# Optimization experiments

Measured on AMD Instinct MI355X. Metric: run time of the kernel, lower is better.

Reference implementation:

```python
import jax, jax.numpy as jnp
import numpy as np
from jax import lax

EPS = 1e-5
K = 16  # MixedOp.self.k


def conv(x, w, stride=1, pad=0, dil=1, groups=1):
    return lax.conv_general_dilated(
        x, w, (stride, stride), [(pad, pad), (pad, pad)],
        rhs_dilation=(dil, dil), feature_group_count=groups,
        dimension_numbers=('NCHW', 'OIHW', 'NCHW'))


def bn(x):
    # BatchNorm2d(affine=False) in training mode: normalize with batch stats
    m = jnp.mean(x, axis=(0, 2, 3), keepdims=True)
    v = jnp.var(x, axis=(0, 2, 3), keepdims=True)
    return (x - m) * lax.rsqrt(v + EPS)


def maxpool3(x):
    return lax.reduce_window(x, -jnp.inf, lax.max, (1, 1, 3, 3), (1, 1, 1, 1),
                             [(0, 0), (0, 0), (1, 1), (1, 1)])


def avgpool3(x):
    # AvgPool2d(3, stride=1, padding=1, count_include_pad=False)
    s = lax.reduce_window(x, 0., lax.add, (1, 1, 3, 3), (1, 1, 1, 1),
                          [(0, 0), (0, 0), (1, 1), (1, 1)])
    c = lax.reduce_window(jnp.ones_like(x), 0., lax.add, (1, 1, 3, 3),
                          (1, 1, 1, 1), [(0, 0), (0, 0), (1, 1), (1, 1)])
    return s / c


def sep_conv(x, dw1, pw1, dw2, pw2):
    C = x.shape[1]
    p = dw1.shape[-1] // 2
    h = jax.nn.relu(x)
    h = conv(h, dw1, pad=p, groups=C)
    h = bn(conv(h, pw1))
    h = jax.nn.relu(h)
    h = conv(h, dw2, pad=p, groups=C)
    return bn(conv(h, pw2))


def dil_conv(x, dw, pw):
    C = x.shape[1]
    p = (dw.shape[-1] // 2) * 2  # dilation=2 padding (3x3->2, 5x5->4)
    h = jax.nn.relu(x)
    h = conv(h, dw, pad=p, dil=2, groups=C)
    return bn(conv(h, pw))


def setup_inputs() -> dict:
    key = jax.random.key(0)
    C, B, H, W = 256, 32, 64, 64
    c_op = C // K  # 16 channels fed to each candidate op
    ks = jax.random.split(key, 17)
    g = lambda k, shp, fan: jax.random.normal(k, shp, jnp.float32) / np.sqrt(fan)
    return {
        'x': jax.random.normal(ks[0], (B, C, H, W), jnp.float32),
        # ChannelAttention se: 1x1 convs, reduction=2
        'ca_w1': g(ks[1], (C // 2, C, 1, 1), C),
        'ca_w2': g(ks[2], (C, C // 2, 1, 1), C // 2),
        # sep_conv_3x3 (two dw+pw stages)
        's3_dw1': g(ks[3], (c_op, 1, 3, 3), 9),
        's3_pw1': g(ks[4], (c_op, c_op, 1, 1), c_op),
        's3_dw2': g(ks[5], (c_op, 1, 3, 3), 9),
        's3_pw2': g(ks[6], (c_op, c_op, 1, 1), c_op),
        # sep_conv_5x5
        's5_dw1': g(ks[7], (c_op, 1, 5, 5), 25),
        's5_pw1': g(ks[8], (c_op, c_op, 1, 1), c_op),
        's5_dw2': g(ks[9], (c_op, 1, 5, 5), 25),
        's5_pw2': g(ks[10], (c_op, c_op, 1, 1), c_op),
        # dil_conv_3x3 / dil_conv_5x5
        'd3_dw': g(ks[11], (c_op, 1, 3, 3), 9),
        'd3_pw': g(ks[12], (c_op, c_op, 1, 1), c_op),
        'd5_dw': g(ks[13], (c_op, 1, 5, 5), 25),
        'd5_pw': g(ks[14], (c_op, c_op, 1, 1), c_op),
        # AttentionModule fc: channel = 8*c_op = 128, ratio = 8
        'at_w1': g(ks[15], (c_op, 8 * c_op), 8 * c_op),  # Linear(128->16)
        'at_w2': g(ks[16], (8 * c_op, c_op), c_op),      # Linear(16->128)
    }


def reference(x, ca_w1, ca_w2, s3_dw1, s3_pw1, s3_dw2, s3_pw2,
              s5_dw1, s5_pw1, s5_dw2, s5_pw2, d3_dw, d3_pw, d5_dw, d5_pw,
              at_w1, at_w2):
    B, C, H, W = x.shape
    c_sel = C // K  # number of selected channels (16)

    # ---- ChannelAttention ----
    mx = jnp.max(x, axis=(2, 3), keepdims=True)   # [B,C,1,1]
    av = jnp.mean(x, axis=(2, 3), keepdims=True)
    se = lambda z: conv(jax.nn.relu(conv(z, ca_w1)), ca_w2)
    num_list = jax.nn.sigmoid(se(mx) + se(av))    # [B,C,1,1]

    aux = x                                       # auxiliary_op = Identity (stride=1)
    xg = x * num_list

    # ---- top-k channel routing ----
    slist = jnp.sum(num_list, axis=0).reshape(C)  # sum over batch
    _, idx = lax.top_k(slist, c_sel)              # sorted, largest first
    xt = xg[:, idx]                               # gather [B,c_sel,H,W]

    # ---- 8 candidate branches (DARTS PRIMITIVES, stride=1) ----
    branches = [
        jnp.zeros_like(xt),                       # none
        bn(maxpool3(xt)),                         # max_pool_3x3 + BN
        bn(avgpool3(xt)),                         # avg_pool_3x3 + BN
        xt,                                       # skip_connect (Identity)
        sep_conv(xt, s3_dw1, s3_pw1, s3_dw2, s3_pw2),
        sep_conv(xt, s5_dw1, s5_pw1, s5_dw2, s5_pw2),
        dil_conv(xt, d3_dw, d3_pw),
        dil_conv(xt, d5_dw, d5_pw),
    ]
    temp = jnp.concatenate(branches, axis=1)      # [B, 8*c_sel, H, W]

    # ---- AttentionModule ----
    y = jnp.mean(temp, axis=(2, 3))               # [B, 8*c_sel]
    y = jax.nn.sigmoid(jax.nn.relu(y @ at_w1.T) @ at_w2.T)
    att = temp * y[:, :, None, None]
    op_attention = jnp.sum(y.reshape(B, 8, c_sel), axis=(0, 2))  # [8]

    # sum the 8 branch chunks
    out = jnp.sum(att.reshape(B, 8, c_sel, H, W), axis=1)

    # scatter back into gated x, then residual add
    xg = xg.at[:, idx].set(out)
    return xg + aux, op_attention
```

## Files before the change

### kernel.cpp

```cpp
#include <hip/hip_runtime.h>
#include <math.h>

static constexpr int B = 32, C = 256, HW = 4096, CS = 16;
static constexpr int BHW = B * HW;
static constexpr size_t IMG = (size_t)B * CS * HW;

static constexpr size_t OFF_S    = 0;
static constexpr size_t OFF_SQ   = 4096;
static constexpr size_t OFF_U    = 8192;
static constexpr size_t OFF_CNT  = 8256;
static constexpr size_t ACC_END  = 8260;
static constexpr size_t OFF_MX   = 8320;
static constexpr size_t OFF_AV   = OFF_MX + 8192;
static constexpr size_t OFF_NUM  = OFF_AV + 8192;
static constexpr size_t OFF_Y    = OFF_NUM + 8192;
static constexpr size_t OFF_ACO  = OFF_Y + 4096;
static constexpr size_t OFF_BIAS = OFF_ACO + 4096;
static constexpr size_t OFF_INT  = OFF_BIAS + 512;
static constexpr size_t OFF_R    = OFF_INT + 384;

__device__ inline float wave_sum(float v) {
  v += __shfl_down(v, 32); v += __shfl_down(v, 16); v += __shfl_down(v, 8);
  v += __shfl_down(v, 4);  v += __shfl_down(v, 2);  v += __shfl_down(v, 1);
  return v;
}
__device__ inline float wave_max(float v) {
  v = fmaxf(v, __shfl_down(v, 32)); v = fmaxf(v, __shfl_down(v, 16));
  v = fmaxf(v, __shfl_down(v, 8));  v = fmaxf(v, __shfl_down(v, 4));
  v = fmaxf(v, __shfl_down(v, 2));  v = fmaxf(v, __shfl_down(v, 1));
  return v;
}

__global__ __launch_bounds__(256) void k_stats(const float4* __restrict__ x,
                                               float* __restrict__ mx, float* __restrict__ av,
                                               float* __restrict__ accbase) {
  int bc = blockIdx.x;
  if (bc == 0) for (int i = threadIdx.x; i < (int)ACC_END; i += 256) accbase[i] = 0.f;
  const float4* p = x + (size_t)bc * 1024;
  float mmax = -INFINITY, msum = 0.f;
  for (int i = threadIdx.x; i < 1024; i += 256) {
    float4 v = p[i];
    mmax = fmaxf(mmax, fmaxf(fmaxf(v.x, v.y), fmaxf(v.z, v.w)));
    msum += v.x + v.y + v.z + v.w;
  }
  __shared__ float rs[4], rm[4];
  float s = wave_sum(msum), m = wave_max(mmax);
  int w = threadIdx.x >> 6;
  if ((threadIdx.x & 63) == 0) { rs[w] = s; rm[w] = m; }
  __syncthreads();
  if (threadIdx.x == 0) {
    mx[bc] = fmaxf(fmaxf(rm[0], rm[1]), fmaxf(rm[2], rm[3]));
    av[bc] = (rs[0] + rs[1] + rs[2] + rs[3]) * (1.f / 4096.f);
  }
}

__global__ __launch_bounds__(256) void k_sesel(const float* __restrict__ mx, const float* __restrict__ av,
                                               const float* __restrict__ w1, const float* __restrict__ w2,
                                               float* __restrict__ num,
                                               int* __restrict__ idx, int* __restrict__ selmap,
                                               unsigned* __restrict__ cnt) {
  __shared__ float zs0[256], zs1[256], h0[128], h1[128];
  __shared__ unsigned lastv;
  int b = blockIdx.x, t = threadIdx.x;
  zs0[t] = mx[b * 256 + t]; zs1[t] = av[b * 256 + t];
  __syncthreads();
  if (t < 128) {
    const float* wr = w1 + (size_t)t * 256;
    float am = 0.f, aa = 0.f;
    for (int i = 0; i < 256; i++) { float w = wr[i]; am = fmaf(w, zs0[i], am); aa = fmaf(w, zs1[i], aa); }
    h0[t] = fmaxf(am, 0.f); h1[t] = fmaxf(aa, 0.f);
  }
  __syncthreads();
  {
    const float* wr = w2 + (size_t)t * 128;
    float sm = 0.f, sa = 0.f;
    for (int j = 0; j < 128; j++) { float w = wr[j]; sm = fmaf(w, h0[j], sm); sa = fmaf(w, h1[j], sa); }
    num[b * 256 + t] = 1.f / (1.f + expf(-(sm + sa)));
  }
  __threadfence();
  if (t == 0) lastv = atomicAdd(cnt, 1u);
  __syncthreads();
  if (lastv == 31u) {
    __threadfence();
    float acc = 0.f;
    for (int bb = 0; bb < B; bb++) acc += num[bb * 256 + t];
    zs0[t] = acc; selmap[t] = -1;
    __syncthreads();
    float v = zs0[t];
    int rank = 0;
    for (int c = 0; c < 256; c++) {
      float o = zs0[c];
      rank += (o > v) || (o == v && c < t);
    }
    if (rank < 16) { idx[rank] = t; selmap[t] = rank; }
  }
}

__global__ __launch_bounds__(256) void k_fuseA(
    const float* __restrict__ x, const float* __restrict__ num, const int* __restrict__ idx,
    const float* __restrict__ d3dw, const float* __restrict__ d5dw,
    const float* __restrict__ s3dw1, const float* __restrict__ s5dw1,
    float* __restrict__ R, float* __restrict__ scr,
    float* __restrict__ S, float* __restrict__ SQ) {
  __shared__ float lt[72 * 72];
  __shared__ float red[20];
  const int t = threadIdx.x;
  const int bk = blockIdx.x, b = bk >> 4, k = bk & 15;
  const int c = idx[k];
  const float sc = num[b * 256 + c];
  const float* src = x + ((size_t)b * 256 + c) * HW;
  const size_t o = (size_t)bk * HW;
  for (int i = t; i < 72 * 72; i += 256) {
    int ty = i / 72, tx = i - ty * 72;
    int y = ty - 4, xx = tx - 4;
    float v = 0.f;
    if ((unsigned)y < 64u && (unsigned)xx < 64u) v = src[y * 64 + xx] * sc;
    lt[i] = v;
  }
  __syncthreads();
  {
    float s1 = 0.f, q1 = 0.f, s2 = 0.f, q2 = 0.f, s3 = 0.f;
    for (int i = t; i < HW; i += 256) {
      int y = i >> 6, xx = i & 63;
      const float* ctr = lt + (y + 4) * 72 + (xx + 4);
      int dy0 = (y > 0) ? -1 : 0, dy1 = (y < 63) ? 1 : 0;
      int dx0 = (xx > 0) ? -1 : 0, dx1 = (xx < 63) ? 1 : 0;
      float mxv = -INFINITY, sm = 0.f;
      for (int dy = dy0; dy <= dy1; dy++)
        for (int dx = dx0; dx <= dx1; dx++) { float v = ctr[dy * 72 + dx]; mxv = fmaxf(mxv, v); sm += v; }
      float avv = sm / (float)((dy1 - dy0 + 1) * (dx1 - dx0 + 1));
      R[o + i] = mxv; R[IMG + o + i] = avv;
      s1 += mxv; q1 += mxv * mxv; s2 += avv; q2 += avv * avv; s3 += ctr[0];
    }
    s1 = wave_sum(s1); q1 = wave_sum(q1); s2 = wave_sum(s2); q2 = wave_sum(q2); s3 = wave_sum(s3);
    int w = t >> 6;
    if ((t & 63) == 0) { red[w] = s1; red[4 + w] = q1; red[8 + w] = s2; red[12 + w] = q2; red[16 + w] = s3; }
    __syncthreads();
    if (t == 0) {
      S[512 + bk]  = red[0] + red[1] + red[2] + red[3];
      SQ[512 + bk] = red[4] + red[5] + red[6] + red[7];
      S[1024 + bk] = red[8] + red[9] + red[10] + red[11];
      SQ[1024 + bk]= red[12] + red[13] + red[14] + red[15];
      S[1536 + bk] = red[16] + red[17] + red[18] + red[19];
    }
  }
  {
    float w[9];
#pragma unroll
    for (int i = 0; i < 9; i++) w[i] = d3dw[k * 9 + i];
    for (int i = t; i < HW; i += 256) {
      int y = i >> 6, xx = i & 63;
      const float* ctr = lt + (y + 4) * 72 + (xx + 4);
      float acc = 0.f;
#pragma unroll
      for (int a = 0; a < 3; a++)
#pragma unroll
        for (int q = 0; q < 3; q++)
          acc = fmaf(w[a * 3 + q], fmaxf(ctr[(2 * a - 2) * 72 + (2 * q - 2)], 0.f), acc);
      scr[0 * IMG + o + i] = acc;
    }
  }
  {
    float w[25];
#pragma unroll
    for (int i = 0; i < 25; i++) w[i] = d5dw[k * 25 + i];
    for (int i = t; i < HW; i += 256) {
      int y = i >> 6, xx = i & 63;
      const float* ctr = lt + (y + 4) * 72 + (xx + 4);
      float acc = 0.f;
#pragma unroll
      for (int a = 0; a < 5; a++)
#pragma unroll
        for (int q = 0; q < 5; q++)
          acc = fmaf(w[a * 5 + q], fmaxf(ctr[(2 * a - 4) * 72 + (2 * q - 4)], 0.f), acc);
      scr[1 * IMG + o + i] = acc;
    }
  }
  {
    float w[9];
#pragma unroll
    for (int i = 0; i < 9; i++) w[i] = s3dw1[k * 9 + i];
    for (int i = t; i < HW; i += 256) {
      int y = i >> 6, xx = i & 63;
      const float* ctr = lt + (y + 4) * 72 + (xx + 4);
      float acc = 0.f;
#pragma unroll
      for (int a = 0; a < 3; a++)
#pragma unroll
        for (int q = 0; q < 3; q++)
          acc = fmaf(w[a * 3 + q], fmaxf(ctr[(a - 1) * 72 + (q - 1)], 0.f), acc);
      scr[2 * IMG + o + i] = acc;
    }
  }
  {
    float w[25];
#pragma unroll
    for (int i = 0; i < 25; i++) w[i] = s5dw1[k * 25 + i];
    for (int i = t; i < HW; i += 256) {
      int y = i >> 6, xx = i & 63;
      const float* ctr = lt + (y + 4) * 72 + (xx + 4);
      float acc = 0.f;
#pragma unroll
      for (int a = 0; a < 5; a++)
#pragma unroll
        for (int q = 0; q < 5; q++)
          acc = fmaf(w[a * 5 + q], fmaxf(ctr[(a - 2) * 72 + (q - 2)], 0.f), acc);
      scr[3 * IMG + o + i] = acc;
    }
  }
}

__device__ __forceinline__ void do_pw(const float* __restrict__ in, const float* __restrict__ wsh,
                                      float* __restrict__ out, float* __restrict__ sacc,
                                      float* __restrict__ qacc, int perB, int b, int tile,
                                      float* redS, float* redQ) {
  int t = threadIdx.x;
  size_t base = (size_t)b * 16 * HW + tile * 256;
  float sv[16];
#pragma unroll
  for (int i = 0; i < 16; i++) sv[i] = in[base + (size_t)i * HW + t];
  int wv = t >> 6, lane = t & 63;
  __syncthreads();
#pragma unroll
  for (int cc = 0; cc < 16; cc++) {
    float acc = 0.f;
#pragma unroll
    for (int i = 0; i < 16; i++) acc = fmaf(wsh[cc * 16 + i], sv[i], acc);
    out[base + (size_t)cc * HW + t] = acc;
    float s = wave_sum(acc), q = wave_sum(acc * acc);
    if (lane == 0) { redS[cc * 4 + wv] = s; redQ[cc * 4 + wv] = q; }
  }
  __syncthreads();
  if (t < 16) {
    float s = redS[t * 4] + redS[t * 4 + 1] + redS[t * 4 + 2] + redS[t * 4 + 3];
    float q = redQ[t * 4] + redQ[t * 4 + 1] + redQ[t * 4 + 2] + redQ[t * 4 + 3];
    int sl = perB ? b * 16 + t : t;
    atomicAdd(&sacc[sl], s); atomicAdd(&qacc[sl], q);
  }
}

__global__ __launch_bounds__(256) void k_fuseB(
    const float* __restrict__ scr,
    const float* __restrict__ d3pw, const float* __restrict__ d5pw,
    const float* __restrict__ s3pw1, const float* __restrict__ s5pw1,
    float* __restrict__ R, float* __restrict__ t3, float* __restrict__ t5,
    float* __restrict__ S, float* __restrict__ SQ, float* __restrict__ U) {
  __shared__ float wall[1024], redS[64], redQ[64];
  int t = threadIdx.x;
  int b = blockIdx.x >> 4, tile = blockIdx.x & 15;
  wall[t] = d3pw[t]; wall[256 + t] = d5pw[t]; wall[512 + t] = s3pw1[t]; wall[768 + t] = s5pw1[t];
  do_pw(scr + 0 * IMG, wall + 0,   R + 4 * IMG, S + 6 * 512, SQ + 6 * 512, 1, b, tile, redS, redQ);
  do_pw(scr + 1 * IMG, wall + 256, R + 5 * IMG, S + 7 * 512, SQ + 7 * 512, 1, b, tile, redS, redQ);
  do_pw(scr + 2 * IMG, wall + 512, t3, U + 0,  U + 16, 0, b, tile, redS, redQ);
  do_pw(scr + 3 * IMG, wall + 768, t5, U + 32, U + 48, 0, b, tile, redS, redQ);
}

template<int KK, int BN>
__device__ __forceinline__ void dw_one(const float* __restrict__ src, const float* __restrict__ w,
                                       float* __restrict__ dst, float* lt, float mu, float rs) {
  constexpr int P = KK / 2, TW = 64 + 2 * P;
  float wr[KK * KK];
#pragma unroll
  for (int i = 0; i < KK * KK; i++) wr[i] = w[i];
  for (int i = threadIdx.x; i < TW * TW; i += 256) {
    int ty = i / TW, tx = i - ty * TW;
    int y = ty - P, xx = tx - P;
    float v = 0.f;
    if ((unsigned)y < 64u && (unsigned)xx < 64u) {
      v = src[y * 64 + xx];
      if (BN) v = (v - mu) * rs;
      v = fmaxf(v, 0.f);
    }
    lt[i] = v;
  }
  __syncthreads();
  for (int i = threadIdx.x; i < HW; i += 256) {
    int y = i >> 6, xx = i & 63;
    const float* t0 = lt + y * TW + xx;
    float acc = 0.f;
#pragma unroll
    for (int a = 0; a < KK; a++)
#pragma unroll
      for (int q = 0; q < KK; q++)
        acc = fmaf(wr[a * KK + q], t0[a * TW + q], acc);
    dst[i] = acc;
  }
}

__global__ __launch_bounds__(256) void k_fuseC(
    const float* __restrict__ t3, const float* __restrict__ t5,
    const float* __restrict__ s3dw2, const float* __restrict__ s5dw2,
    float* __restrict__ scr, const float* __restrict__ U) {
  __shared__ float lt[68 * 68];
  int blk = blockIdx.x;
  int op = blk >> 9, bk = blk & 511, k = bk & 15;
  size_t o = (size_t)bk * HW;
  if (op == 0) {
    float mu = U[k] * (1.f / (float)BHW);
    float var = U[16 + k] * (1.f / (float)BHW) - mu * mu;
    dw_one<3, 1>(t3 + o, s3dw2 + k * 9, scr + 0 * IMG + o, lt, mu, rsqrtf(var + 1e-5f));
  } else {
    float mu = U[32 + k] * (1.f / (float)BHW);
    float var = U[48 + k] * (1.f / (float)BHW) - mu * mu;
    dw_one<5, 1>(t5 + o, s5dw2 + k * 25, scr + 1 * IMG + o, lt, mu, rsqrtf(var + 1e-5f));
  }
}

__global__ __launch_bounds__(256) void k_fuseD(
    const float* __restrict__ scr,
    const float* __restrict__ s3pw2, const float* __restrict__ s5pw2,
    float* __restrict__ R, float* __restrict__ S, float* __restrict__ SQ) {
  __shared__ float wall[512], redS[64], redQ[64];
  int t = threadIdx.x;
  int b = blockIdx.x >> 4, tile = blockIdx.x & 15;
  wall[t] = s3pw2[t]; wall[256 + t] = s5pw2[t];
  do_pw(scr + 0 * IMG, wall + 0,   R + 2 * IMG, S + 4 * 512, SQ + 4 * 512, 1, b, tile, redS, redQ);
  do_pw(scr + 1 * IMG, wall + 256, R + 3 * IMG, S + 5 * 512, SQ + 5 * 512, 1, b, tile, redS, redQ);
}

__global__ __launch_bounds__(128) void k_att(const float* __restrict__ S, const float* __restrict__ SQ,
                                             const float* __restrict__ w1, const float* __restrict__ w2,
                                             float* __restrict__ y, float* __restrict__ aco,
                                             float* __restrict__ bia) {
  int b = blockIdx.x, t = threadIdx.x;
  __shared__ float ym[128], h[16], msh[8][16], rssh[8][16], ysh[128];
  int op = t >> 4, k = t & 15;
  bool isbn = (op == 1 || op == 2 || op >= 4);
  float m = 0.f, rsc = 0.f;
  {
    float ss = 0.f, qq = 0.f;
    for (int bb = 0; bb < B; bb++) { ss += S[op * 512 + bb * 16 + k]; qq += SQ[op * 512 + bb * 16 + k]; }
    if (isbn) {
      m = ss * (1.f / (float)BHW);
      float var = qq * (1.f / (float)BHW) - m * m;
      rsc = rsqrtf(var + 1e-5f);
    }
  }
  msh[op][k] = m; rssh[op][k] = rsc;
  float sm = S[op * 512 + b * 16 + k] * (1.f / 4096.f);
  float yme = (op == 0) ? 0.f : ((op == 3) ? sm : (sm - m) * rsc);
  ym[t] = yme;
  __syncthreads();
  if (t < 16) {
    const float* wr = w1 + (size_t)t * 128;
    float acc = 0.f;
    for (int c = 0; c < 128; c++) acc = fmaf(wr[c], ym[c], acc);
    h[t] = fmaxf(acc, 0.f);
  }
  __syncthreads();
  {
    const float* wr = w2 + (size_t)t * 16;
    float acc = 0.f;
    for (int j = 0; j < 16; j++) acc = fmaf(wr[j], h[j], acc);
    float yy = 1.f / (1.f + expf(-acc));
    ysh[t] = yy; y[b * 128 + t] = yy;
  }
  __syncthreads();
  if (t < 16) {
    float bias = 0.f;
    for (int o2 = 1; o2 < 8; o2++) {
      float yv = ysh[o2 * 16 + t];
      float a;
      if (o2 == 3) a = yv;
      else { a = yv * rssh[o2][t]; bias -= yv * rssh[o2][t] * msh[o2][t]; }
      aco[(b * 16 + t) * 8 + o2] = a;
    }
    bia[b * 16 + t] = bias;
  }
}

__global__ __launch_bounds__(256) void k_final(const float* __restrict__ x, const float* __restrict__ num,
                                               const int* __restrict__ selmap, const int* __restrict__ idx,
                                               const float* __restrict__ rbuf, const float* __restrict__ aco,
                                               const float* __restrict__ bia, const float* __restrict__ ybuf,
                                               float* __restrict__ out, float* __restrict__ out8) {
  __shared__ float sh[256];
  int bc = blockIdx.x;
  if (bc == B * C) {
    int t = threadIdx.x, op = t >> 5, lane = t & 31;
    float acc = 0.f;
    for (int i = lane; i < 512; i += 32) { int bb = i >> 4, kk = i & 15; acc += ybuf[bb * 128 + op * 16 + kk]; }
    sh[t] = acc;
    __syncthreads();
    if (lane == 0) {
      float s = 0.f;
      for (int i = 0; i < 32; i++) s += sh[op * 32 + i];
      out8[op] = s;
    }
    return;
  }
  int b = bc >> 8;
  int k = selmap[bc & 255];
  const float4* xs = (const float4*)(x + (size_t)bc * HW);
  float4* od = (float4*)(out + (size_t)bc * HW);
  if (k < 0) {
    float sc = 1.f + num[bc];
    for (int i = threadIdx.x; i < 1024; i += 256) {
      float4 v = xs[i];
      v.x *= sc; v.y *= sc; v.z *= sc; v.w *= sc;
      od[i] = v;
    }
  } else {
    int bk = b * 16 + k;
    int ci = idx[k];
    float scn = num[b * 256 + ci];
    const float4* xtp = (const float4*)(x + ((size_t)b * 256 + ci) * HW);
    const float4* r0 = (const float4*)(rbuf + ((size_t)0 * 512 + bk) * HW);
    const float4* r1 = (const float4*)(rbuf + ((size_t)1 * 512 + bk) * HW);
    const float4* r2 = (const float4*)(rbuf + ((size_t)2 * 512 + bk) * HW);
    const float4* r3 = (const float4*)(rbuf + ((size_t)3 * 512 + bk) * HW);
    const float4* r4 = (const float4*)(rbuf + ((size_t)4 * 512 + bk) * HW);
    const float4* r5 = (const float4*)(rbuf + ((size_t)5 * 512 + bk) * HW);
    float a1 = aco[bk * 8 + 1], a2 = aco[bk * 8 + 2], a3 = aco[bk * 8 + 3] * scn, a4 = aco[bk * 8 + 4];
    float a5 = aco[bk * 8 + 5], a6 = aco[bk * 8 + 6], a7 = aco[bk * 8 + 7];
    float bias = bia[bk];
    for (int i = threadIdx.x; i < 1024; i += 256) {
      float4 xv = xs[i], tv = xtp[i];
      float4 v0 = r0[i], v1 = r1[i], v2 = r2[i], v3 = r3[i], v4 = r4[i], v5 = r5[i];
      float4 o;
      o.x = xv.x + bias + a1 * v0.x + a2 * v1.x + a3 * tv.x + a4 * v2.x + a5 * v3.x + a6 * v4.x + a7 * v5.x;
      o.y = xv.y + bias + a1 * v0.y + a2 * v1.y + a3 * tv.y + a4 * v2.y + a5 * v3.y + a6 * v4.y + a7 * v5.y;
      o.z = xv.z + bias + a1 * v0.z + a2 * v1.z + a3 * tv.z + a4 * v2.z + a5 * v3.z + a6 * v4.z + a7 * v5.z;
      o.w = xv.w + bias + a1 * v0.w + a2 * v1.w + a3 * tv.w + a4 * v2.w + a5 * v3.w + a6 * v4.w + a7 * v5.w;
      od[i] = o;
    }
  }
}

extern "C" void kernel_launch(void* const* d_in, const int* in_sizes, int n_in,
                              void* d_out, int out_size, void* d_ws, size_t ws_size,
                              hipStream_t stream) {
  const float* x      = (const float*)d_in[0];
  const float* ca_w1  = (const float*)d_in[1];
  const float* ca_w2  = (const float*)d_in[2];
  const float* s3_dw1 = (const float*)d_in[3];
  const float* s3_pw1 = (const float*)d_in[4];
  const float* s3_dw2 = (const float*)d_in[5];
  const float* s3_pw2 = (const float*)d_in[6];
  const float* s5_dw1 = (const float*)d_in[7];
  const float* s5_pw1 = (const float*)d_in[8];
  const float* s5_dw2 = (const float*)d_in[9];
  const float* s5_pw2 = (const float*)d_in[10];
  const float* d3_dw  = (const float*)d_in[11];
  const float* d3_pw  = (const float*)d_in[12];
  const float* d5_dw  = (const float*)d_in[13];
  const float* d5_pw  = (const float*)d_in[14];
  const float* at_w1  = (const float*)d_in[15];
  const float* at_w2  = (const float*)d_in[16];

  float* ws = (float*)d_ws;
  float* S = ws + OFF_S;  float* SQ = ws + OFF_SQ;  float* U = ws + OFF_U;
  unsigned* cnt = (unsigned*)(ws + OFF_CNT);
  float* mx = ws + OFF_MX; float* av = ws + OFF_AV; float* num = ws + OFF_NUM;
  float* ybuf = ws + OFF_Y; float* aco = ws + OFF_ACO; float* bia = ws + OFF_BIAS;
  int* ib = (int*)(ws + OFF_INT);
  int* idx = ib; int* selmap = ib + 16;
  float* R = ws + OFF_R;

  float* outf = (float*)d_out;
  float* scr = outf;
  float* t3  = outf + 4 * IMG;
  float* t5  = outf + 5 * IMG;
  float* out8 = outf + (size_t)B * C * HW;

  k_stats<<<B * C, 256, 0, stream>>>((const float4*)x, mx, av, ws);
  k_sesel<<<B, 256, 0, stream>>>(mx, av, ca_w1, ca_w2, num, idx, selmap, cnt);
  k_fuseA<<<512, 256, 0, stream>>>(x, num, idx, d3_dw, d5_dw, s3_dw1, s5_dw1, R, scr, S, SQ);
  k_fuseB<<<512, 256, 0, stream>>>(scr, d3_pw, d5_pw, s3_pw1, s5_pw1, R, t3, t5, S, SQ, U);
  k_fuseC<<<2 * 512, 256, 0, stream>>>(t3, t5, s3_dw2, s5_dw2, scr, U);
  k_fuseD<<<512, 256, 0, stream>>>(scr, s3_pw2, s5_pw2, R, S, SQ);
  k_att<<<B, 128, 0, stream>>>(S, SQ, at_w1, at_w2, ybuf, aco, bia);
  k_final<<<B * C + 1, 256, 0, stream>>>(x, num, selmap, idx, R, aco, bia, ybuf, outf, out8);
}
```

Baseline: 218.4 us.

## Split depthwise and pointwise stages into row-quarter blocks with float4 pointwise

Measured after the change: 199.9 us. 8.5% less time.

```diff
diff --git a/kernel.cpp b/kernel.cpp
--- a/kernel.cpp
+++ b/kernel.cpp
@@ -102,17 +102,20 @@
     const float* __restrict__ s3dw1, const float* __restrict__ s5dw1,
     float* __restrict__ R, float* __restrict__ scr,
     float* __restrict__ S, float* __restrict__ SQ) {
-  __shared__ float lt[72 * 72];
+  __shared__ float lt[24 * 72];
   __shared__ float red[20];
   const int t = threadIdx.x;
-  const int bk = blockIdx.x, b = bk >> 4, k = bk & 15;
+  const int blk = blockIdx.x;
+  const int bk = blk >> 2, qt = blk & 3;
+  const int b = bk >> 4, k = bk & 15;
   const int c = idx[k];
   const float sc = num[b * 256 + c];
   const float* src = x + ((size_t)b * 256 + c) * HW;
-  const size_t o = (size_t)bk * HW;
-  for (int i = t; i < 72 * 72; i += 256) {
+  const size_t o = (size_t)bk * HW + qt * 1024;
+  const int ry0 = qt * 16;
+  for (int i = t; i < 24 * 72; i += 256) {
     int ty = i / 72, tx = i - ty * 72;
-    int y = ty - 4, xx = tx - 4;
+    int y = ry0 - 4 + ty, xx = tx - 4;
     float v = 0.f;
     if ((unsigned)y < 64u && (unsigned)xx < 64u) v = src[y * 64 + xx] * sc;
     lt[i] = v;
@@ -120,11 +123,12 @@
   __syncthreads();
   {
     float s1 = 0.f, q1 = 0.f, s2 = 0.f, q2 = 0.f, s3 = 0.f;
-    for (int i = t; i < HW; i += 256) {
-      int y = i >> 6, xx = i & 63;
-      const float* ctr = lt + (y + 4) * 72 + (xx + 4);
+    for (int i = t; i < 1024; i += 256) {
+      int lr = i >> 6, col = i & 63;
+      int y = ry0 + lr;
+      const float* ctr = lt + (lr + 4) * 72 + (col + 4);
       int dy0 = (y > 0) ? -1 : 0, dy1 = (y < 63) ? 1 : 0;
-      int dx0 = (xx > 0) ? -1 : 0, dx1 = (xx < 63) ? 1 : 0;
+      int dx0 = (col > 0) ? -1 : 0, dx1 = (col < 63) ? 1 : 0;
       float mxv = -INFINITY, sm = 0.f;
       for (int dy = dy0; dy <= dy1; dy++)
         for (int dx = dx0; dx <= dx1; dx++) { float v = ctr[dy * 72 + dx]; mxv = fmaxf(mxv, v); sm += v; }
@@ -137,20 +141,20 @@
     if ((t & 63) == 0) { red[w] = s1; red[4 + w] = q1; red[8 + w] = s2; red[12 + w] = q2; red[16 + w] = s3; }
     __syncthreads();
     if (t == 0) {
-      S[512 + bk]  = red[0] + red[1] + red[2] + red[3];
-      SQ[512 + bk] = red[4] + red[5] + red[6] + red[7];
-      S[1024 + bk] = red[8] + red[9] + red[10] + red[11];
-      SQ[1024 + bk]= red[12] + red[13] + red[14] + red[15];
-      S[1536 + bk] = red[16] + red[17] + red[18] + red[19];
+      atomicAdd(&S[512 + bk],   red[0] + red[1] + red[2] + red[3]);
+      atomicAdd(&SQ[512 + bk],  red[4] + red[5] + red[6] + red[7]);
+      atomicAdd(&S[1024 + bk],  red[8] + red[9] + red[10] + red[11]);
+      atomicAdd(&SQ[1024 + bk], red[12] + red[13] + red[14] + red[15]);
+      atomicAdd(&S[1536 + bk],  red[16] + red[17] + red[18] + red[19]);
     }
   }
   {
     float w[9];
 #pragma unroll
     for (int i = 0; i < 9; i++) w[i] = d3dw[k * 9 + i];
-    for (int i = t; i < HW; i += 256) {
-      int y = i >> 6, xx = i & 63;
-      const float* ctr = lt + (y + 4) * 72 + (xx + 4);
+    for (int i = t; i < 1024; i += 256) {
+      int lr = i >> 6, col = i & 63;
+      const float* ctr = lt + (lr + 4) * 72 + (col + 4);
       float acc = 0.f;
 #pragma unroll
       for (int a = 0; a < 3; a++)
@@ -164,9 +168,9 @@
     float w[25];
 #pragma unroll
     for (int i = 0; i < 25; i++) w[i] = d5dw[k * 25 + i];
-    for (int i = t; i < HW; i += 256) {
-      int y = i >> 6, xx = i & 63;
-      const float* ctr = lt + (y + 4) * 72 + (xx + 4);
+    for (int i = t; i < 1024; i += 256) {
+      int lr = i >> 6, col = i & 63;
+      const float* ctr = lt + (lr + 4) * 72 + (col + 4);
       float acc = 0.f;
 #pragma unroll
       for (int a = 0; a < 5; a++)
@@ -180,9 +184,9 @@
     float w[9];
 #pragma unroll
     for (int i = 0; i < 9; i++) w[i] = s3dw1[k * 9 + i];
-    for (int i = t; i < HW; i += 256) {
-      int y = i >> 6, xx = i & 63;
-      const float* ctr = lt + (y + 4) * 72 + (xx + 4);
+    for (int i = t; i < 1024; i += 256) {
+      int lr = i >> 6, col = i & 63;
+      const float* ctr = lt + (lr + 4) * 72 + (col + 4);
       float acc = 0.f;
 #pragma unroll
       for (int a = 0; a < 3; a++)
@@ -196,9 +200,9 @@
     float w[25];
 #pragma unroll
     for (int i = 0; i < 25; i++) w[i] = s5dw1[k * 25 + i];
-    for (int i = t; i < HW; i += 256) {
-      int y = i >> 6, xx = i & 63;
-      const float* ctr = lt + (y + 4) * 72 + (xx + 4);
+    for (int i = t; i < 1024; i += 256) {
+      int lr = i >> 6, col = i & 63;
+      const float* ctr = lt + (lr + 4) * 72 + (col + 4);
       float acc = 0.f;
 #pragma unroll
       for (int a = 0; a < 5; a++)
@@ -210,25 +214,32 @@
   }
 }
 
-__device__ __forceinline__ void do_pw(const float* __restrict__ in, const float* __restrict__ wsh,
-                                      float* __restrict__ out, float* __restrict__ sacc,
-                                      float* __restrict__ qacc, int perB, int b, int tile,
-                                      float* redS, float* redQ) {
+__device__ __forceinline__ void pw4(const float* __restrict__ in, const float* __restrict__ w16,
+                                    float* __restrict__ out, float* __restrict__ sacc,
+                                    float* __restrict__ qacc, int perB, int b, int q4,
+                                    float* wsh, float* redS, float* redQ) {
   int t = threadIdx.x;
-  size_t base = (size_t)b * 16 * HW + tile * 256;
-  float sv[16];
-#pragma unroll
-  for (int i = 0; i < 16; i++) sv[i] = in[base + (size_t)i * HW + t];
+  wsh[t] = w16[t];
+  size_t base = (size_t)b * 16 * HW + q4 * 1024 + t * 4;
+  float4 sv[16];
+#pragma unroll
+  for (int i = 0; i < 16; i++) sv[i] = *(const float4*)(in + base + (size_t)i * HW);
+  __syncthreads();
   int wv = t >> 6, lane = t & 63;
-  __syncthreads();
 #pragma unroll
   for (int cc = 0; cc < 16; cc++) {
-    float acc = 0.f;
-#pragma unroll
-    for (int i = 0; i < 16; i++) acc = fmaf(wsh[cc * 16 + i], sv[i], acc);
-    out[base + (size_t)cc * HW + t] = acc;
-    float s = wave_sum(acc), q = wave_sum(acc * acc);
-    if (lane == 0) { redS[cc * 4 + wv] = s; redQ[cc * 4 + wv] = q; }
+    float4 o; o.x = 0.f; o.y = 0.f; o.z = 0.f; o.w = 0.f;
+#pragma unroll
+    for (int i = 0; i < 16; i++) {
+      float w = wsh[cc * 16 + i];
+      o.x = fmaf(w, sv[i].x, o.x); o.y = fmaf(w, sv[i].y, o.y);
+      o.z = fmaf(w, sv[i].z, o.z); o.w = fmaf(w, sv[i].w, o.w);
+    }
+    *(float4*)(out + base + (size_t)cc * HW) = o;
+    float s = (o.x + o.y) + (o.z + o.w);
+    float qv = fmaf(o.x, o.x, fmaf(o.y, o.y, fmaf(o.z, o.z, o.w * o.w)));
+    s = wave_sum(s); qv = wave_sum(qv);
+    if (lane == 0) { redS[cc * 4 + wv] = s; redQ[cc * 4 + wv] = qv; }
   }
   __syncthreads();
   if (t < 16) {
@@ -245,45 +256,49 @@
     const float* __restrict__ s3pw1, const float* __restrict__ s5pw1,
     float* __restrict__ R, float* __restrict__ t3, float* __restrict__ t5,
     float* __restrict__ S, float* __restrict__ SQ, float* __restrict__ U) {
-  __shared__ float wall[1024], redS[64], redQ[64];
-  int t = threadIdx.x;
-  int b = blockIdx.x >> 4, tile = blockIdx.x & 15;
-  wall[t] = d3pw[t]; wall[256 + t] = d5pw[t]; wall[512 + t] = s3pw1[t]; wall[768 + t] = s5pw1[t];
-  do_pw(scr + 0 * IMG, wall + 0,   R + 4 * IMG, S + 6 * 512, SQ + 6 * 512, 1, b, tile, redS, redQ);
-  do_pw(scr + 1 * IMG, wall + 256, R + 5 * IMG, S + 7 * 512, SQ + 7 * 512, 1, b, tile, redS, redQ);
-  do_pw(scr + 2 * IMG, wall + 512, t3, U + 0,  U + 16, 0, b, tile, redS, redQ);
-  do_pw(scr + 3 * IMG, wall + 768, t5, U + 32, U + 48, 0, b, tile, redS, redQ);
-}
-
-template<int KK, int BN>
-__device__ __forceinline__ void dw_one(const float* __restrict__ src, const float* __restrict__ w,
-                                       float* __restrict__ dst, float* lt, float mu, float rs) {
-  constexpr int P = KK / 2, TW = 64 + 2 * P;
+  __shared__ float wsh[256], redS[64], redQ[64];
+  int blk = blockIdx.x;
+  int op = blk >> 7, rem = blk & 127;
+  int b = rem >> 2, q4 = rem & 3;
+  switch (op) {
+    case 0: pw4(scr + 0 * IMG, d3pw,  R + 4 * IMG, S + 6 * 512, SQ + 6 * 512, 1, b, q4, wsh, redS, redQ); break;
+    case 1: pw4(scr + 1 * IMG, d5pw,  R + 5 * IMG, S + 7 * 512, SQ + 7 * 512, 1, b, q4, wsh, redS, redQ); break;
+    case 2: pw4(scr + 2 * IMG, s3pw1, t3, U + 0,  U + 16, 0, b, q4, wsh, redS, redQ); break;
+    case 3: pw4(scr + 3 * IMG, s5pw1, t5, U + 32, U + 48, 0, b, q4, wsh, redS, redQ); break;
+  }
+}
+
+template<int KK>
+__device__ __forceinline__ void dw_q(const float* __restrict__ src, const float* __restrict__ w,
+                                     float* __restrict__ dst, float* lt, float mu, float rs, int qt) {
+  constexpr int P = KK / 2, TW = 64 + 2 * P, ROWS = 16 + 2 * P;
   float wr[KK * KK];
 #pragma unroll
   for (int i = 0; i < KK * KK; i++) wr[i] = w[i];
-  for (int i = threadIdx.x; i < TW * TW; i += 256) {
+  const int t = threadIdx.x;
+  const int ry0 = qt * 16;
+  for (int i = t; i < ROWS * TW; i += 256) {
     int ty = i / TW, tx = i - ty * TW;
-    int y = ty - P, xx = tx - P;
+    int y = ry0 - P + ty, xx = tx - P;
     float v = 0.f;
     if ((unsigned)y < 64u && (unsigned)xx < 64u) {
       v = src[y * 64 + xx];
-      if (BN) v = (v - mu) * rs;
+      v = (v - mu) * rs;
       v = fmaxf(v, 0.f);
     }
     lt[i] = v;
   }
   __syncthreads();
-  for (int i = threadIdx.x; i < HW; i += 256) {
-    int y = i >> 6, xx = i & 63;
-    const float* t0 = lt + y * TW + xx;
+  for (int i = t; i < 1024; i += 256) {
+    int lr = i >> 6, col = i & 63;
+    const float* t0 = lt + lr * TW + col;
     float acc = 0.f;
 #pragma unroll
     for (int a = 0; a < KK; a++)
 #pragma unroll
       for (int q = 0; q < KK; q++)
         acc = fmaf(wr[a * KK + q], t0[a * TW + q], acc);
-    dst[i] = acc;
+    dst[qt * 1024 + i] = acc;
   }
 }
 
@@ -291,18 +306,19 @@
     const float* __restrict__ t3, const float* __restrict__ t5,
     const float* __restrict__ s3dw2, const float* __restrict__ s5dw2,
     float* __restrict__ scr, const float* __restrict__ U) {
-  __shared__ float lt[68 * 68];
+  __shared__ float lt[20 * 68];
   int blk = blockIdx.x;
-  int op = blk >> 9, bk = blk & 511, k = bk & 15;
+  int op = blk >> 11, rem = blk & 2047;
+  int bk = rem >> 2, qt = rem & 3, k = bk & 15;
   size_t o = (size_t)bk * HW;
   if (op == 0) {
     float mu = U[k] * (1.f / (float)BHW);
     float var = U[16 + k] * (1.f / (float)BHW) - mu * mu;
-    dw_one<3, 1>(t3 + o, s3dw2 + k * 9, scr + 0 * IMG + o, lt, mu, rsqrtf(var + 1e-5f));
+    dw_q<3>(t3 + o, s3dw2 + k * 9, scr + 0 * IMG + o, lt, mu, rsqrtf(var + 1e-5f), qt);
   } else {
     float mu = U[32 + k] * (1.f / (float)BHW);
     float var = U[48 + k] * (1.f / (float)BHW) - mu * mu;
-    dw_one<5, 1>(t5 + o, s5dw2 + k * 25, scr + 1 * IMG + o, lt, mu, rsqrtf(var + 1e-5f));
+    dw_q<5>(t5 + o, s5dw2 + k * 25, scr + 1 * IMG + o, lt, mu, rsqrtf(var + 1e-5f), qt);
   }
 }
 
@@ -310,12 +326,12 @@
     const float* __restrict__ scr,
     const float* __restrict__ s3pw2, const float* __restrict__ s5pw2,
     float* __restrict__ R, float* __restrict__ S, float* __restrict__ SQ) {
-  __shared__ float wall[512], redS[64], redQ[64];
-  int t = threadIdx.x;
-  int b = blockIdx.x >> 4, tile = blockIdx.x & 15;
-  wall[t] = s3pw2[t]; wall[256 + t] = s5pw2[t];
-  do_pw(scr + 0 * IMG, wall + 0,   R + 2 * IMG, S + 4 * 512, SQ + 4 * 512, 1, b, tile, redS, redQ);
-  do_pw(scr + 1 * IMG, wall + 256, R + 3 * IMG, S + 5 * 512, SQ + 5 * 512, 1, b, tile, redS, redQ);
+  __shared__ float wsh[256], redS[64], redQ[64];
+  int blk = blockIdx.x;
+  int op = blk >> 7, rem = blk & 127;
+  int b = rem >> 2, q4 = rem & 3;
+  if (op == 0) pw4(scr + 0 * IMG, s3pw2, R + 2 * IMG, S + 4 * 512, SQ + 4 * 512, 1, b, q4, wsh, redS, redQ);
+  else         pw4(scr + 1 * IMG, s5pw2, R + 3 * IMG, S + 5 * 512, SQ + 5 * 512, 1, b, q4, wsh, redS, redQ);
 }
 
 __global__ __launch_bounds__(128) void k_att(const float* __restrict__ S, const float* __restrict__ SQ,
@@ -465,10 +481,10 @@
 
   k_stats<<<B * C, 256, 0, stream>>>((const float4*)x, mx, av, ws);
   k_sesel<<<B, 256, 0, stream>>>(mx, av, ca_w1, ca_w2, num, idx, selmap, cnt);
-  k_fuseA<<<512, 256, 0, stream>>>(x, num, idx, d3_dw, d5_dw, s3_dw1, s5_dw1, R, scr, S, SQ);
+  k_fuseA<<<2048, 256, 0, stream>>>(x, num, idx, d3_dw, d5_dw, s3_dw1, s5_dw1, R, scr, S, SQ);
   k_fuseB<<<512, 256, 0, stream>>>(scr, d3_pw, d5_pw, s3_pw1, s5_pw1, R, t3, t5, S, SQ, U);
-  k_fuseC<<<2 * 512, 256, 0, stream>>>(t3, t5, s3_dw2, s5_dw2, scr, U);
-  k_fuseD<<<512, 256, 0, stream>>>(scr, s3_pw2, s5_pw2, R, S, SQ);
+  k_fuseC<<<4096, 256, 0, stream>>>(t3, t5, s3_dw2, s5_dw2, scr, U);
+  k_fuseD<<<256, 256, 0, stream>>>(scr, s3_pw2, s5_pw2, R, S, SQ);
   k_att<<<B, 128, 0, stream>>>(S, SQ, at_w1, at_w2, ybuf, aco, bia);
   k_final<<<B * C + 1, 256, 0, stream>>>(x, num, selmap, idx, R, aco, bia, ybuf, outf, out8);
 }
```
